# Optimization experiments

Hardware: AMD Instinct MI355X
Metric: run time of the kernel (lower is better)

## Reference

```python
import jax, jax.numpy as jnp
import numpy as np

N_NODES = 100000
NFEAT, NHID, NCLASS = 256, 128, 40
N_EDGES = 1600000


def setup_inputs() -> dict:
    key = jax.random.key(0)
    ks = jax.random.split(key, 12)
    x = jax.random.normal(ks[0], (N_NODES, NFEAT), dtype=jnp.float32)
    edge_index = jax.random.randint(ks[1], (2, N_EDGES), 0, N_NODES, dtype=jnp.int32)
    def lin(kw, kb, fan_in, fan_out):
        bound = 1.0 / np.sqrt(fan_in)
        W = jax.random.uniform(kw, (fan_in, fan_out), minval=-bound, maxval=bound, dtype=jnp.float32)
        b = jax.random.uniform(kb, (fan_out,), minval=-bound, maxval=bound, dtype=jnp.float32)
        return W, b
    W_pre, b_pre = lin(ks[2], ks[3], NFEAT, NHID)
    W1, b1 = lin(ks[4], ks[5], NHID, NHID)
    W2, b2 = lin(ks[6], ks[7], NHID, NHID)
    W_post, b_post = lin(ks[8], ks[9], NHID, NCLASS)
    return {"x": x, "edge_index": edge_index,
            "W_pre": W_pre, "b_pre": b_pre,
            "W1": W1, "b1": b1, "W2": W2, "b2": b2,
            "W_post": W_post, "b_post": b_post}


def _gcn_norm(edge_index, num_nodes):
    # add self-loops, symmetric normalization (PyG GCNConv default)
    loops = jnp.arange(num_nodes, dtype=edge_index.dtype)
    src = jnp.concatenate([edge_index[0], loops])  # [E+N]
    dst = jnp.concatenate([edge_index[1], loops])
    deg = jax.ops.segment_sum(jnp.ones_like(dst, dtype=jnp.float32), dst, num_segments=num_nodes)
    dinv = jnp.where(deg > 0, jax.lax.rsqrt(deg), 0.0)
    norm = dinv[src] * dinv[dst]  # [E+N]
    return src, dst, norm


def _gcn_conv(h, W, b, src, dst, norm, num_nodes):
    h = h @ W                                   # [N, out]
    msg = h[src] * norm[:, None]                # gather + scale, [E+N, out]
    out = jax.ops.segment_sum(msg, dst, num_segments=num_nodes)  # scatter-add
    return out + b


def reference(x, edge_index, W_pre, b_pre, W1, b1, W2, b2, W_post, b_post):
    n = x.shape[0]
    src, dst, norm = _gcn_norm(edge_index, n)
    h = x @ W_pre + b_pre
    h = jax.nn.relu(_gcn_conv(h, W1, b1, src, dst, norm, n))
    h = jax.nn.relu(_gcn_conv(h, W2, b2, src, dst, norm, n))
    h = h @ W_post + b_post
    return jax.nn.log_softmax(h, axis=1)
```

## Files before the change

### kernel.cpp

```cpp
#include <hip/hip_runtime.h>
#include <hip/hip_bf16.h>


#define NFEAT 256
#define NHID  128
#define NCLASS 40

#define BSH   9
#define CHUNK 8192

typedef __attribute__((ext_vector_type(8))) __bf16 bf16x8;
typedef __attribute__((ext_vector_type(4))) float f32x4;
typedef __attribute__((ext_vector_type(8))) unsigned short ushort8;

__device__ __forceinline__ unsigned short f2bf(float f) {
    unsigned int u = __builtin_bit_cast(unsigned int, f);
    u = (u + 0x7FFF + ((u >> 16) & 1)) >> 16;
    return (unsigned short)u;
}
__device__ __forceinline__ float bf2f(unsigned short h) {
    unsigned int u = ((unsigned int)h) << 16;
    return __builtin_bit_cast(float, u);
}


__global__ __launch_bounds__(256) void bucket_count(const int* __restrict__ dst,
                                                    int* __restrict__ bcnt, int E, int nbk) {
    __shared__ int h[256];
    int tid = threadIdx.x;
    h[tid] = 0;
    __syncthreads();
    for (int e = blockIdx.x * 256 + tid; e < E; e += gridDim.x * 256)
        atomicAdd(&h[dst[e] >> BSH], 1);
    __syncthreads();
    if (tid < nbk && h[tid]) atomicAdd(&bcnt[tid], h[tid]);
}

__global__ __launch_bounds__(256) void bucket_scan(const int* __restrict__ bcnt,
                                                   int* __restrict__ boff,
                                                   int* __restrict__ bcur, int nbk, int E) {
    __shared__ int s[256];
    int tid = threadIdx.x;
    int v = (tid < nbk) ? bcnt[tid] : 0;
    s[tid] = v;
    __syncthreads();
    for (int off = 1; off < 256; off <<= 1) {
        int t = (tid >= off) ? s[tid - off] : 0;
        __syncthreads();
        s[tid] += t;
        __syncthreads();
    }
    if (tid < nbk) { int ex = s[tid] - v; boff[tid] = ex; bcur[tid] = ex; }
    if (tid == 0) boff[nbk] = E;
}

__global__ __launch_bounds__(256) void bucket_scatter(const int* __restrict__ src,
                                                      const int* __restrict__ dst,
                                                      int* __restrict__ bcur,
                                                      uint2* __restrict__ ebuf, int E, int nbk) {
    __shared__ uint2 pairs[CHUNK];
    __shared__ int lcnt[256], lpos[256], delta[256], s[256];
    int tid = threadIdx.x;
    int base = blockIdx.x * CHUNK;
    int cnt = min(CHUNK, E - base);
    lcnt[tid] = 0;
    __syncthreads();
    for (int i = tid; i < cnt; i += 256)
        atomicAdd(&lcnt[dst[base + i] >> BSH], 1);
    __syncthreads();
    int v = lcnt[tid];
    s[tid] = v;
    __syncthreads();
    for (int off = 1; off < 256; off <<= 1) {
        int t = (tid >= off) ? s[tid - off] : 0;
        __syncthreads();
        s[tid] += t;
        __syncthreads();
    }
    lpos[tid] = s[tid] - v;
    if (tid < nbk && v) {
        int gb = atomicAdd(&bcur[tid], v);
        delta[tid] = gb - (s[tid] - v);
    }
    lcnt[tid] = 0;
    __syncthreads();
    for (int i = tid; i < cnt; i += 256) {
        int d = dst[base + i], sv = src[base + i];
        int b = d >> BSH;
        int idx = lpos[b] + atomicAdd(&lcnt[b], 1);
        pairs[idx] = make_uint2((unsigned)sv, (unsigned)d);
    }
    __syncthreads();
    for (int i = tid; i < cnt; i += 256) {
        uint2 p = pairs[i];
        ebuf[delta[p.y >> BSH] + i] = p;
    }
}

__global__ __launch_bounds__(512) void csr_finalize(const uint2* __restrict__ ebuf,
                                                    const int* __restrict__ boff,
                                                    int* __restrict__ rowptr,
                                                    float* __restrict__ dinv,
                                                    int* __restrict__ col, int N, int E) {
    __shared__ int cnt[512], s[512];
    int tid = threadIdx.x;
    int b = blockIdx.x;
    int d0 = b << BSH;
    int beg = boff[b], end = boff[b + 1];
    cnt[tid] = 0;
    __syncthreads();
    for (int j = beg + tid; j < end; j += 512)
        atomicAdd(&cnt[ebuf[j].y - d0], 1);
    __syncthreads();
    int v = cnt[tid];
    s[tid] = v;
    __syncthreads();
    for (int off = 1; off < 512; off <<= 1) {
        int t = (tid >= off) ? s[tid - off] : 0;
        __syncthreads();
        s[tid] += t;
        __syncthreads();
    }
    int ex = s[tid] - v;
    int d = d0 + tid;
    if (d < N) {
        rowptr[d] = beg + ex;
        dinv[d] = rsqrtf((float)(v + 1));
    }
    if (b == 0 && tid == 0) rowptr[N] = E;
    __syncthreads();
    cnt[tid] = ex;
    __syncthreads();
    for (int j = beg + tid; j < end; j += 512) {
        uint2 p = ebuf[j];
        int pos = beg + atomicAdd(&cnt[p.y - d0], 1);
        col[pos] = (int)p.x;
    }
}


__global__ void prep_weights(const float* __restrict__ Wpre, const float* __restrict__ W1,
                             const float* __restrict__ W2, const float* __restrict__ Wp,
                             unsigned short* __restrict__ WpreT,
                             unsigned short* __restrict__ W1T,
                             unsigned short* __restrict__ W2T,
                             unsigned short* __restrict__ WpT) {
    int id = blockIdx.x * blockDim.x + threadIdx.x;
    if (id < 32768) {
        int k = id >> 7, c = id & 127;
        WpreT[c * 256 + k] = f2bf(Wpre[id]);
    } else if (id < 49152) {
        int t = id - 32768; int k = t >> 7, c = t & 127;
        W1T[c * 128 + k] = f2bf(W1[t]);
    } else if (id < 65536) {
        int t = id - 49152; int k = t >> 7, c = t & 127;
        W2T[c * 128 + k] = f2bf(W2[t]);
    } else if (id < 71680) {
        int t = id - 65536; int c = t >> 7, k = t & 127;
        WpT[c * 128 + k] = (c < 40) ? f2bf(Wp[k * 40 + c]) : (unsigned short)0;
    }
}


template <int K, bool AFLOAT, bool BIAS>
__global__ __launch_bounds__(256) void gemm_mfma(const void* __restrict__ Av,
                                                 const unsigned short* __restrict__ Wt,
                                                 const float* __restrict__ bias,
                                                 unsigned short* __restrict__ out,
                                                 int N) {
    __shared__ unsigned short Ws[128 * 136];
    int tid = threadIdx.x;
    int lane = tid & 63;
    int w = tid >> 6;
    int l15 = lane & 15;
    int lk = lane >> 4;
    int wrow = blockIdx.x * 128 + w * 32;

    f32x4 acc[2][8];
    #pragma unroll
    for (int mt = 0; mt < 2; mt++)
        #pragma unroll
        for (int nt = 0; nt < 8; nt++)
            acc[mt][nt] = (f32x4)0.f;

    #pragma unroll
    for (int c = 0; c < K / 128; ++c) {
        __syncthreads();
        #pragma unroll
        for (int i = 0; i < 8; i++) {
            int v = tid + i * 256;
            int rowc = v >> 4, c16 = v & 15;
            *(ushort8*)&Ws[rowc * 136 + c16 * 8] =
                *(const ushort8*)&Wt[(size_t)rowc * K + c * 128 + c16 * 8];
        }
        __syncthreads();

        bf16x8 af[2][4];
        #pragma unroll
        for (int mt = 0; mt < 2; mt++) {
            int r = wrow + mt * 16 + l15;
            bool ok = r < N;
            #pragma unroll
            for (int ks = 0; ks < 4; ks++) {
                int k = c * 128 + ks * 32 + lk * 8;
                if (AFLOAT) {
                    const float* ap = (const float*)Av + (size_t)r * K + k;
                    float4 x0 = make_float4(0.f, 0.f, 0.f, 0.f), x1 = x0;
                    if (ok) { x0 = *(const float4*)ap; x1 = *(const float4*)(ap + 4); }
                    ushort8 u;
                    u[0] = f2bf(x0.x); u[1] = f2bf(x0.y); u[2] = f2bf(x0.z); u[3] = f2bf(x0.w);
                    u[4] = f2bf(x1.x); u[5] = f2bf(x1.y); u[6] = f2bf(x1.z); u[7] = f2bf(x1.w);
                    af[mt][ks] = __builtin_bit_cast(bf16x8, u);
                } else {
                    const unsigned short* ap = (const unsigned short*)Av + (size_t)r * K + k;
                    ushort8 u = {};
                    if (ok) u = *(const ushort8*)ap;
                    af[mt][ks] = __builtin_bit_cast(bf16x8, u);
                }
            }
        }

        #pragma unroll
        for (int nt = 0; nt < 8; nt++) {
            bf16x8 bfr[4];
            #pragma unroll
            for (int ks = 0; ks < 4; ks++) {
                ushort8 u = *(const ushort8*)&Ws[(nt * 16 + l15) * 136 + ks * 32 + lk * 8];
                bfr[ks] = __builtin_bit_cast(bf16x8, u);
            }
            #pragma unroll
            for (int ks = 0; ks < 4; ks++) {
                acc[0][nt] = __builtin_amdgcn_mfma_f32_16x16x32_bf16(af[0][ks], bfr[ks], acc[0][nt], 0, 0, 0);
                acc[1][nt] = __builtin_amdgcn_mfma_f32_16x16x32_bf16(af[1][ks], bfr[ks], acc[1][nt], 0, 0, 0);
            }
        }
    }

    #pragma unroll
    for (int nt = 0; nt < 8; nt++) {
        int colc = nt * 16 + l15;
        float bv = BIAS ? bias[colc] : 0.f;
        #pragma unroll
        for (int mt = 0; mt < 2; mt++) {
            #pragma unroll
            for (int j = 0; j < 4; j++) {
                int r = wrow + mt * 16 + lk * 4 + j;
                if (r < N)
                    out[(size_t)r * 128 + colc] = f2bf(acc[mt][nt][j] + bv);
            }
        }
    }
}


__global__ __launch_bounds__(256) void aggregate_bf16(const unsigned short* __restrict__ t,
                                                      const int* __restrict__ rowptr,
                                                      const int* __restrict__ col,
                                                      const float* __restrict__ dinv,
                                                      const float* __restrict__ bias,
                                                      unsigned short* __restrict__ out,
                                                      int N) {
    int gid = blockIdx.x * blockDim.x + threadIdx.x;
    int wid = gid >> 6;
    if (wid >= N) return;
    int lane = threadIdx.x & 63;
    int g  = lane >> 4;
    int sl = lane & 15;

    float dv = dinv[wid];
    int beg = rowptr[wid], end = rowptr[wid + 1];

    float acc[8];
    #pragma unroll
    for (int i = 0; i < 8; i++) acc[i] = 0.f;

    if (g == 0) {
        ushort8 s = *(const ushort8*)&t[(size_t)wid * 128 + sl * 8];
        float w0 = dv * dv;
        #pragma unroll
        for (int i = 0; i < 8; i++) acc[i] = w0 * bf2f(s[i]);
    }

    int e = beg + g;
    int u0 = (e < end) ? col[e] : 0;
    int u1 = (e + 4 < end) ? col[e + 4] : 0;
    while (e < end) {
        float du0 = dinv[u0];
        ushort8 m0 = *(const ushort8*)&t[(size_t)u0 * 128 + sl * 8];
        float du1 = dinv[u1];
        ushort8 m1 = *(const ushort8*)&t[(size_t)u1 * 128 + sl * 8];
        int u2 = (e + 8  < end) ? col[e + 8]  : 0;
        int u3 = (e + 12 < end) ? col[e + 12] : 0;
        float w0 = du0 * dv;
        #pragma unroll
        for (int i = 0; i < 8; i++) acc[i] += w0 * bf2f(m0[i]);
        float w1 = (e + 4 < end) ? du1 * dv : 0.f;
        #pragma unroll
        for (int i = 0; i < 8; i++) acc[i] += w1 * bf2f(m1[i]);
        u0 = u2; u1 = u3;
        e += 8;
    }

    #pragma unroll
    for (int i = 0; i < 8; i++) {
        acc[i] += __shfl_xor(acc[i], 16);
        acc[i] += __shfl_xor(acc[i], 32);
    }

    if (g == 0) {
        float4 b0 = *(const float4*)&bias[sl * 8];
        float4 b1 = *(const float4*)&bias[sl * 8 + 4];
        float bb[8] = {b0.x, b0.y, b0.z, b0.w, b1.x, b1.y, b1.z, b1.w};
        ushort8 o;
        #pragma unroll
        for (int i = 0; i < 8; i++) o[i] = f2bf(fmaxf(acc[i] + bb[i], 0.f));
        *(ushort8*)&out[(size_t)wid * 128 + sl * 8] = o;
    }
}


__global__ __launch_bounds__(256) void post_mfma(const unsigned short* __restrict__ Xb,
                                                 const unsigned short* __restrict__ WpT,
                                                 const float* __restrict__ bp,
                                                 float* __restrict__ out, int N) {
    int tid = threadIdx.x;
    int lane = tid & 63;
    int w = tid >> 6;
    int l15 = lane & 15;
    int lk = lane >> 4;
    int wrow = blockIdx.x * 128 + w * 32;

    bf16x8 bfr[3][4];
    #pragma unroll
    for (int nt = 0; nt < 3; nt++)
        #pragma unroll
        for (int ks = 0; ks < 4; ks++)
            bfr[nt][ks] = __builtin_bit_cast(bf16x8,
                *(const ushort8*)&WpT[(size_t)(nt * 16 + l15) * 128 + ks * 32 + lk * 8]);

    float bv[3];
    #pragma unroll
    for (int nt = 0; nt < 3; nt++) {
        int c = nt * 16 + l15;
        bv[nt] = (c < NCLASS) ? bp[c] : 0.f;
    }

    f32x4 acc[2][3];
    #pragma unroll
    for (int mt = 0; mt < 2; mt++)
        #pragma unroll
        for (int nt = 0; nt < 3; nt++)
            acc[mt][nt] = (f32x4)0.f;

    #pragma unroll
    for (int mt = 0; mt < 2; mt++) {
        int r = wrow + mt * 16 + l15;
        bool ok = r < N;
        #pragma unroll
        for (int ks = 0; ks < 4; ks++) {
            ushort8 u = {};
            if (ok) u = *(const ushort8*)&Xb[(size_t)r * 128 + ks * 32 + lk * 8];
            bf16x8 af = __builtin_bit_cast(bf16x8, u);
            #pragma unroll
            for (int nt = 0; nt < 3; nt++)
                acc[mt][nt] = __builtin_amdgcn_mfma_f32_16x16x32_bf16(af, bfr[nt][ks], acc[mt][nt], 0, 0, 0);
        }
    }

    bool v2 = l15 < 8;
    #pragma unroll
    for (int mt = 0; mt < 2; mt++) {
        #pragma unroll
        for (int j = 0; j < 4; j++) {
            float a0 = acc[mt][0][j] + bv[0];
            float a1 = acc[mt][1][j] + bv[1];
            float a2 = v2 ? (acc[mt][2][j] + bv[2]) : -1e30f;
            float m = fmaxf(fmaxf(a0, a1), a2);
            m = fmaxf(m, __shfl_xor(m, 1));
            m = fmaxf(m, __shfl_xor(m, 2));
            m = fmaxf(m, __shfl_xor(m, 4));
            m = fmaxf(m, __shfl_xor(m, 8));
            float s = __expf(a0 - m) + __expf(a1 - m) + (v2 ? __expf(a2 - m) : 0.f);
            s += __shfl_xor(s, 1);
            s += __shfl_xor(s, 2);
            s += __shfl_xor(s, 4);
            s += __shfl_xor(s, 8);
            float lse = m + __logf(s);
            int r = wrow + mt * 16 + lk * 4 + j;
            if (r < N) {
                out[(size_t)r * 40 + l15]      = a0 - lse;
                out[(size_t)r * 40 + 16 + l15] = a1 - lse;
                if (v2) out[(size_t)r * 40 + 32 + l15] = a2 - lse;
            }
        }
    }
}


extern "C" void kernel_launch(void* const* d_in, const int* in_sizes, int n_in,
                              void* d_out, int out_size, void* d_ws, size_t ws_size,
                              hipStream_t stream) {
    const int N = in_sizes[0] / NFEAT;
    const int E = in_sizes[1] / 2;
    const int nbk = (N + (1 << BSH) - 1) >> BSH;

    const float* x     = (const float*)d_in[0];
    const int*   ei    = (const int*)d_in[1];
    const int*   src   = ei;
    const int*   dst   = ei + E;
    const float* W_pre = (const float*)d_in[2];
    const float* b_pre = (const float*)d_in[3];
    const float* W1    = (const float*)d_in[4];
    const float* b1    = (const float*)d_in[5];
    const float* W2    = (const float*)d_in[6];
    const float* b2    = (const float*)d_in[7];
    const float* Wp    = (const float*)d_in[8];
    const float* bp    = (const float*)d_in[9];
    float* out = (float*)d_out;

    char* ws = (char*)d_ws;
    size_t off = 0;
    auto alloc = [&](size_t bytes) -> void* {
        off = (off + 255) & ~(size_t)255;
        void* p = ws + off;
        off += bytes;
        return p;
    };
    int*   rowptr  = (int*)alloc((size_t)(N + 1) * 4);
    float* dinv    = (float*)alloc((size_t)N * 4);
    int*   colbuf  = (int*)alloc((size_t)E * 4);
    uint2* ebuf    = (uint2*)alloc((size_t)E * 8);
    int*   bcnt    = (int*)alloc(256 * 4);
    int*   boff    = (int*)alloc(257 * 4);
    int*   bcur    = (int*)alloc(256 * 4);
    unsigned short* WpreT = (unsigned short*)alloc((size_t)NFEAT * NHID * 2);
    unsigned short* W1T   = (unsigned short*)alloc((size_t)NHID * NHID * 2);
    unsigned short* W2T   = (unsigned short*)alloc((size_t)NHID * NHID * 2);
    unsigned short* WpT   = (unsigned short*)alloc((size_t)48 * NHID * 2);
    unsigned short* bufA  = (unsigned short*)alloc((size_t)N * NHID * 2);
    unsigned short* bufB  = (unsigned short*)alloc((size_t)N * NHID * 2);
    (void)ws_size;

    int gsc = (E + CHUNK - 1) / CHUNK;
    int gm  = (N + 127) / 128;
    int ga  = (int)(((size_t)N * 64 + 255) / 256);

    hipMemsetAsync(bcnt, 0, 256 * 4, stream);
    bucket_count<<<128, 256, 0, stream>>>(dst, bcnt, E, nbk);
    bucket_scan<<<1, 256, 0, stream>>>(bcnt, boff, bcur, nbk, E);
    bucket_scatter<<<gsc, 256, 0, stream>>>(src, dst, bcur, ebuf, E, nbk);
    csr_finalize<<<nbk, 512, 0, stream>>>(ebuf, boff, rowptr, dinv, colbuf, N, E);
    prep_weights<<<280, 256, 0, stream>>>(W_pre, W1, W2, Wp, WpreT, W1T, W2T, WpT);

    gemm_mfma<NFEAT, true, true><<<gm, 256, 0, stream>>>(x, WpreT, b_pre, bufA, N);

    gemm_mfma<NHID, false, false><<<gm, 256, 0, stream>>>(bufA, W1T, nullptr, bufB, N);
    aggregate_bf16<<<ga, 256, 0, stream>>>(bufB, rowptr, colbuf, dinv, b1, bufA, N);

    gemm_mfma<NHID, false, false><<<gm, 256, 0, stream>>>(bufA, W2T, nullptr, bufB, N);
    aggregate_bf16<<<ga, 256, 0, stream>>>(bufB, rowptr, colbuf, dinv, b2, bufA, N);

    post_mfma<<<gm, 256, 0, stream>>>(bufA, WpT, bp, out, N);
}
```

Baseline: 436.2 us.

## Fold pre-linear into first GCN weight and swizzle GEMM LDS with staged stores

Precomputes Wc = W_pre·W1 and bc = b_pre·W1 in a small kernel, so the input is multiplied once by a 256x128 combined weight and one full N×128 GEMM pass, with its bf16 intermediate round-trip, is removed. The GEMM shared-memory tile for weights now uses an XOR swizzle instead of padding to avoid bank conflicts. Output is staged through shared memory so rows are written with 16-byte vector stores rather than scattered 2-byte stores. Float A loads are issued all at once before conversion to overlap memory latency. Numerics change slightly because the combined weight is rounded to bf16 once instead of rounding the intermediate activations.

```diff
diff --git a/kernel.cpp b/kernel.cpp
--- a/kernel.cpp
+++ b/kernel.cpp
@@ -139,24 +139,47 @@
 }
 
 
-__global__ void prep_weights(const float* __restrict__ Wpre, const float* __restrict__ W1,
-                             const float* __restrict__ W2, const float* __restrict__ Wp,
-                             unsigned short* __restrict__ WpreT,
-                             unsigned short* __restrict__ W1T,
+__global__ __launch_bounds__(256) void fuse_weights(const float* __restrict__ Wpre,
+                                                    const float* __restrict__ W1,
+                                                    const float* __restrict__ bpre,
+                                                    unsigned short* __restrict__ WcT,
+                                                    float* __restrict__ bc) {
+    __shared__ unsigned short W1s[128 * 128];
+    int tid = threadIdx.x;
+    for (int i = tid; i < 4096; i += 256) {
+        float4 a = ((const float4*)W1)[i];
+        W1s[i * 4 + 0] = f2bf(a.x);
+        W1s[i * 4 + 1] = f2bf(a.y);
+        W1s[i * 4 + 2] = f2bf(a.z);
+        W1s[i * 4 + 3] = f2bf(a.w);
+    }
+    __syncthreads();
+    int b = blockIdx.x;
+    if (b < 128) {
+        int k = b * 2 + (tid >> 7);
+        int c = tid & 127;
+        const float* wrow = Wpre + (size_t)k * 128;
+        float acc = 0.f;
+        #pragma unroll 8
+        for (int j = 0; j < 128; j++) acc += wrow[j] * bf2f(W1s[j * 128 + c]);
+        WcT[c * 256 + k] = f2bf(acc);
+    } else if (tid < 128) {
+        float acc = 0.f;
+        for (int j = 0; j < 128; j++) acc += bpre[j] * bf2f(W1s[j * 128 + tid]);
+        bc[tid] = acc;
+    }
+}
+
+
+__global__ void prep_weights(const float* __restrict__ W2, const float* __restrict__ Wp,
                              unsigned short* __restrict__ W2T,
                              unsigned short* __restrict__ WpT) {
     int id = blockIdx.x * blockDim.x + threadIdx.x;
-    if (id < 32768) {
+    if (id < 16384) {
         int k = id >> 7, c = id & 127;
-        WpreT[c * 256 + k] = f2bf(Wpre[id]);
-    } else if (id < 49152) {
-        int t = id - 32768; int k = t >> 7, c = t & 127;
-        W1T[c * 128 + k] = f2bf(W1[t]);
-    } else if (id < 65536) {
-        int t = id - 49152; int k = t >> 7, c = t & 127;
-        W2T[c * 128 + k] = f2bf(W2[t]);
-    } else if (id < 71680) {
-        int t = id - 65536; int c = t >> 7, k = t & 127;
+        W2T[c * 128 + k] = f2bf(W2[id]);
+    } else if (id < 22528) {
+        int t = id - 16384; int c = t >> 7, k = t & 127;
         WpT[c * 128 + k] = (c < 40) ? f2bf(Wp[k * 40 + c]) : (unsigned short)0;
     }
 }
@@ -168,7 +191,7 @@
                                                  const float* __restrict__ bias,
                                                  unsigned short* __restrict__ out,
                                                  int N) {
-    __shared__ unsigned short Ws[128 * 136];
+    __shared__ unsigned short Ws[16384];
     int tid = threadIdx.x;
     int lane = tid & 63;
     int w = tid >> 6;
@@ -190,7 +213,8 @@
         for (int i = 0; i < 8; i++) {
             int v = tid + i * 256;
             int rowc = v >> 4, c16 = v & 15;
-            *(ushort8*)&Ws[rowc * 136 + c16 * 8] =
+            int byte = (rowc * 256 + c16 * 16) ^ ((rowc & 7) << 4);
+            *(ushort8*)((char*)Ws + byte) =
                 *(const ushort8*)&Wt[(size_t)rowc * K + c * 128 + c16 * 8];
         }
         __syncthreads();
@@ -200,21 +224,30 @@
         for (int mt = 0; mt < 2; mt++) {
             int r = wrow + mt * 16 + l15;
             bool ok = r < N;
-            #pragma unroll
-            for (int ks = 0; ks < 4; ks++) {
-                int k = c * 128 + ks * 32 + lk * 8;
-                if (AFLOAT) {
-                    const float* ap = (const float*)Av + (size_t)r * K + k;
-                    float4 x0 = make_float4(0.f, 0.f, 0.f, 0.f), x1 = x0;
-                    if (ok) { x0 = *(const float4*)ap; x1 = *(const float4*)(ap + 4); }
+            if (AFLOAT) {
+                float4 raw[4][2];
+                const float* ap0 = (const float*)Av + (size_t)r * K + c * 128 + lk * 8;
+                float4 z = make_float4(0.f, 0.f, 0.f, 0.f);
+                #pragma unroll
+                for (int ks = 0; ks < 4; ks++) {
+                    raw[ks][0] = ok ? *(const float4*)(ap0 + ks * 32) : z;
+                    raw[ks][1] = ok ? *(const float4*)(ap0 + ks * 32 + 4) : z;
+                }
+                #pragma unroll
+                for (int ks = 0; ks < 4; ks++) {
                     ushort8 u;
-                    u[0] = f2bf(x0.x); u[1] = f2bf(x0.y); u[2] = f2bf(x0.z); u[3] = f2bf(x0.w);
-                    u[4] = f2bf(x1.x); u[5] = f2bf(x1.y); u[6] = f2bf(x1.z); u[7] = f2bf(x1.w);
+                    u[0] = f2bf(raw[ks][0].x); u[1] = f2bf(raw[ks][0].y);
+                    u[2] = f2bf(raw[ks][0].z); u[3] = f2bf(raw[ks][0].w);
+                    u[4] = f2bf(raw[ks][1].x); u[5] = f2bf(raw[ks][1].y);
+                    u[6] = f2bf(raw[ks][1].z); u[7] = f2bf(raw[ks][1].w);
                     af[mt][ks] = __builtin_bit_cast(bf16x8, u);
-                } else {
-                    const unsigned short* ap = (const unsigned short*)Av + (size_t)r * K + k;
+                }
+            } else {
+                const unsigned short* ap = (const unsigned short*)Av + (size_t)r * K + c * 128 + lk * 8;
+                #pragma unroll
+                for (int ks = 0; ks < 4; ks++) {
                     ushort8 u = {};
-                    if (ok) u = *(const ushort8*)ap;
+                    if (ok) u = *(const ushort8*)(ap + ks * 32);
                     af[mt][ks] = __builtin_bit_cast(bf16x8, u);
                 }
             }
@@ -225,8 +258,9 @@
             bf16x8 bfr[4];
             #pragma unroll
             for (int ks = 0; ks < 4; ks++) {
-                ushort8 u = *(const ushort8*)&Ws[(nt * 16 + l15) * 136 + ks * 32 + lk * 8];
-                bfr[ks] = __builtin_bit_cast(bf16x8, u);
+                int row = nt * 16 + l15;
+                int byte = (row * 256 + ks * 64 + lk * 16) ^ ((row & 7) << 4);
+                bfr[ks] = *(bf16x8*)((char*)Ws + byte);
             }
             #pragma unroll
             for (int ks = 0; ks < 4; ks++) {
@@ -236,19 +270,29 @@
         }
     }
 
-    #pragma unroll
-    for (int nt = 0; nt < 8; nt++) {
-        int colc = nt * 16 + l15;
-        float bv = BIAS ? bias[colc] : 0.f;
-        #pragma unroll
-        for (int mt = 0; mt < 2; mt++) {
+    __syncthreads();
+    unsigned short* scr = Ws + w * 2176;
+    int srow = lane >> 2;
+    int bch  = lane & 3;
+    #pragma unroll
+    for (int mt = 0; mt < 2; mt++) {
+        #pragma unroll
+        for (int nt = 0; nt < 8; nt++) {
+            float bv = BIAS ? bias[nt * 16 + l15] : 0.f;
             #pragma unroll
-            for (int j = 0; j < 4; j++) {
-                int r = wrow + mt * 16 + lk * 4 + j;
-                if (r < N)
-                    out[(size_t)r * 128 + colc] = f2bf(acc[mt][nt][j] + bv);
-            }
-        }
+            for (int j = 0; j < 4; j++)
+                scr[(lk * 4 + j) * 136 + nt * 16 + l15] = f2bf(acc[mt][nt][j] + bv);
+        }
+        __syncthreads();
+        int grow = wrow + mt * 16 + srow;
+        #pragma unroll
+        for (int it = 0; it < 4; it++) {
+            int chunk = bch + it * 4;
+            ushort8 v = *(ushort8*)&scr[srow * 136 + chunk * 8];
+            if (grow < N)
+                *(ushort8*)&out[(size_t)grow * 128 + chunk * 8] = v;
+        }
+        __syncthreads();
     }
 }
 
@@ -433,12 +477,12 @@
     int*   bcnt    = (int*)alloc(256 * 4);
     int*   boff    = (int*)alloc(257 * 4);
     int*   bcur    = (int*)alloc(256 * 4);
-    unsigned short* WpreT = (unsigned short*)alloc((size_t)NFEAT * NHID * 2);
-    unsigned short* W1T   = (unsigned short*)alloc((size_t)NHID * NHID * 2);
-    unsigned short* W2T   = (unsigned short*)alloc((size_t)NHID * NHID * 2);
-    unsigned short* WpT   = (unsigned short*)alloc((size_t)48 * NHID * 2);
-    unsigned short* bufA  = (unsigned short*)alloc((size_t)N * NHID * 2);
-    unsigned short* bufB  = (unsigned short*)alloc((size_t)N * NHID * 2);
+    unsigned short* WcT  = (unsigned short*)alloc((size_t)NFEAT * NHID * 2);
+    float*          bc   = (float*)alloc(128 * 4);
+    unsigned short* W2T  = (unsigned short*)alloc((size_t)NHID * NHID * 2);
+    unsigned short* WpT  = (unsigned short*)alloc((size_t)48 * NHID * 2);
+    unsigned short* bufA = (unsigned short*)alloc((size_t)N * NHID * 2);
+    unsigned short* bufB = (unsigned short*)alloc((size_t)N * NHID * 2);
     (void)ws_size;
 
     int gsc = (E + CHUNK - 1) / CHUNK;
@@ -450,11 +494,11 @@
     bucket_scan<<<1, 256, 0, stream>>>(bcnt, boff, bcur, nbk, E);
     bucket_scatter<<<gsc, 256, 0, stream>>>(src, dst, bcur, ebuf, E, nbk);
     csr_finalize<<<nbk, 512, 0, stream>>>(ebuf, boff, rowptr, dinv, colbuf, N, E);
-    prep_weights<<<280, 256, 0, stream>>>(W_pre, W1, W2, Wp, WpreT, W1T, W2T, WpT);
-
-    gemm_mfma<NFEAT, true, true><<<gm, 256, 0, stream>>>(x, WpreT, b_pre, bufA, N);
-
-    gemm_mfma<NHID, false, false><<<gm, 256, 0, stream>>>(bufA, W1T, nullptr, bufB, N);
+    fuse_weights<<<129, 256, 0, stream>>>(W_pre, W1, b_pre, WcT, bc);
+    prep_weights<<<88, 256, 0, stream>>>(W2, Wp, W2T, WpT);
+
+    gemm_mfma<NFEAT, true, true><<<gm, 256, 0, stream>>>(x, WcT, bc, bufB, N);
+
     aggregate_bf16<<<ga, 256, 0, stream>>>(bufB, rowptr, colbuf, dinv, b1, bufA, N);
 
     gemm_mfma<NHID, false, false><<<gm, 256, 0, stream>>>(bufA, W2T, nullptr, bufB, N);
```

Measured after the change: 421.1 us. -3.4%, faster.
